# Optimization experiments

Measured on AMD Instinct MI355X. Metric: run time of the kernel, lower is better.

## Reference

```python
import jax, jax.numpy as jnp
import numpy as np
from jax import lax

PRE_NMS_THRESH = 0.05
PRE_NMS_TOP_N = 1000
FINAL_NMS_THRESH = 0.4  # hardcoded in forward(): boxlist_nms(..., 0.4)
MIN_SIZE = 0
STRIDE = 4.0
NEG = -1e9

N, C, H, W = 32, 1, 384, 384


def setup_inputs() -> dict:
    key = jax.random.key(0)
    k1, k2 = jax.random.split(key)
    box_cls = jax.random.uniform(k1, (N, C, H, W), dtype=jnp.float32)
    box_regression = jax.random.normal(k2, (N, 4, H, W), dtype=jnp.float32) * 20.0
    image_sizes = jnp.full((N, 2), H * int(STRIDE), dtype=jnp.int32)
    return {"box_cls": box_cls, "box_regression": box_regression, "image_sizes": image_sizes}


def decode_boxes(quad):
    # quad: [N, 4, H, W]; EAST geometry decode at stride 4 -> xyxy
    n, _, h, w = quad.shape
    x = (jnp.arange(w, dtype=quad.dtype) * STRIDE)[None, :]   # [1, W]
    y = (jnp.arange(h, dtype=quad.dtype) * STRIDE)[:, None]   # [H, 1]
    ymin = y - quad[:, 0]
    xmax = x + quad[:, 1]
    ymax = y + quad[:, 2]
    xmin = x - quad[:, 3]
    return jnp.stack([xmin, ymin, xmax, ymax], axis=1)  # [N, 4, H, W] (permute (3,0,1,2))


def iou_matrix(b):
    # b: [K, 4] xyxy
    x1, y1, x2, y2 = b[:, 0], b[:, 1], b[:, 2], b[:, 3]
    area = jnp.clip(x2 - x1, 0) * jnp.clip(y2 - y1, 0)
    ix1 = jnp.maximum(x1[:, None], x1[None, :])
    iy1 = jnp.maximum(y1[:, None], y1[None, :])
    ix2 = jnp.minimum(x2[:, None], x2[None, :])
    iy2 = jnp.minimum(y2[:, None], y2[None, :])
    inter = jnp.clip(ix2 - ix1, 0) * jnp.clip(iy2 - iy1, 0)
    union = area[:, None] + area[None, :] - inter
    return inter / jnp.maximum(union, 1e-9)


def greedy_nms(boxes, init_keep):
    # boxes: [K, 4] sorted by descending score; init_keep: [K] bool
    K = boxes.shape[0]
    iou = iou_matrix(boxes)
    idx = jnp.arange(K)

    def body(i, keep):
        suppress = (iou[i] > FINAL_NMS_THRESH) & (idx > i)
        return jnp.where(keep[i], keep & ~suppress, keep)

    return lax.fori_loop(0, K, body, init_keep)


def _forward(box_cls, box_regression):
    n, c, h, w = box_cls.shape
    boxes = decode_boxes(box_regression)                       # [N, 4, H, W]
    boxes = boxes.transpose(0, 2, 3, 1).reshape(n, h * w, 4)   # [N, HW, 4]
    scores = box_cls.transpose(0, 2, 3, 1).reshape(n, h * w)   # [N, HW] (C=1)

    # threshold + conditional top-k (padding with NEG emulates variable counts)
    masked = jnp.where(scores > PRE_NMS_THRESH, scores, NEG)
    scores_k, idx_k = lax.top_k(masked, PRE_NMS_TOP_N)         # [N, K], sorted desc
    boxes_k = jnp.take_along_axis(boxes, idx_k[..., None], axis=1)  # [N, K, 4]

    valid = scores_k > PRE_NMS_THRESH
    ws = boxes_k[..., 2] - boxes_k[..., 0]
    hs = boxes_k[..., 3] - boxes_k[..., 1]
    valid = valid & (ws >= MIN_SIZE) & (hs >= MIN_SIZE)        # remove_small_boxes

    keep = jax.vmap(greedy_nms)(boxes_k, valid)                # [N, K]
    out = jnp.concatenate([boxes_k, scores_k[..., None]], axis=-1)
    out = out * keep[..., None].astype(out.dtype)              # [N, K, 5]
    return out, keep


def reference(box_cls, box_regression, image_sizes):
    return _forward(box_cls, box_regression)
```

## Files before the change

kernel.cpp:

```cpp
#include <hip/hip_runtime.h>
#include <stdint.h>

#define NIMG 32
#define WID 384
#define HW 147456
#define TOPK 1000
#define KPAD 1024
#define NBINS 512
#define BIN_SCALEF 512.0f
#define SEGCAP 256
#define CANDCAP 2048
#define THRESH 0.05f
#define PREF_C 0.99f
#define NMS_T 0.4f
#define NBLK 18
#define FINEBINS 256

typedef unsigned long long u64;
typedef unsigned int u32;

#define PCNT_OFF 0
#define PCAND_OFF 4096

__device__ __forceinline__ float area_of(float x0, float y0, float x1, float y1) {
  float a = fmaxf(x1 - x0, 0.0f) * fmaxf(y1 - y0, 0.0f);
  asm volatile("" : "+v"(a));
  return a;
}

__device__ __forceinline__ bool iou_gt(float ax0, float ay0, float ax1, float ay1, float aa,
                                       float bx0, float by0, float bx1, float by1, float ba) {
  float ix1 = fmaxf(ax0, bx0);
  float iy1 = fmaxf(ay0, by0);
  float ix2 = fminf(ax1, bx1);
  float iy2 = fminf(ay1, by1);
  float iw = fmaxf(ix2 - ix1, 0.0f);
  float ih = fmaxf(iy2 - iy1, 0.0f);
  float inter = iw * ih;
  asm volatile("" : "+v"(inter));
  float uni = fmaxf(aa + ba - inter, 1e-9f);
  return (inter / uni) > NMS_T;
}

__device__ __forceinline__ u64 shflxor64(u64 v, int m) {
  int lo = __shfl_xor((int)(u32)v, m, 64);
  int hi = __shfl_xor((int)(u32)(v >> 32), m, 64);
  return ((u64)(u32)hi << 32) | (u32)lo;
}

__device__ __forceinline__ u64 make_key(float s, u32 idx) {
  u32 ord = __float_as_uint(s) | 0x80000000u;
  return ((u64)ord << 32) | (u32)(~idx);
}

__device__ __forceinline__ float score_of(u64 key) {
  return __uint_as_float((u32)(key >> 32) & 0x7FFFFFFFu);
}

__device__ __forceinline__ int bin_of(float s) {
  int b = (int)(s * BIN_SCALEF);
  return b < 0 ? 0 : (b > NBINS - 1 ? NBINS - 1 : b);
}

__device__ __forceinline__ int finebin(u64 key) {
  float s = score_of(key);
  int b = (int)((s - 0.99f) * 25600.0f);
  return b < 0 ? 0 : (b > FINEBINS - 1 ? FINEBINS - 1 : b);
}

__global__ __launch_bounds__(256) void scan_kernel(const float* __restrict__ cls,
                                                   u32* __restrict__ pcnt,
                                                   u64* __restrict__ pcand) {
  __shared__ u64 lbuf[SEGCAP];
  __shared__ u32 lcnt;
  const int n = blockIdx.y;
  const int tid = threadIdx.x;
  const int lane = tid & 63;
  if (tid == 0) lcnt = 0;
  __syncthreads();

  const float4* src = (const float4*)(cls + (size_t)n * HW) + blockIdx.x * 2048;
  float4 A[8];
#pragma unroll
  for (int v = 0; v < 8; v++) A[v] = src[tid + v * 256];

  const u64 ltmask = (1ull << lane) - 1ull;
#pragma unroll
  for (int v = 0; v < 8; v++) {
    float ss[4] = {A[v].x, A[v].y, A[v].z, A[v].w};
#pragma unroll
    for (int c = 0; c < 4; c++) {
      float s = ss[c];
      bool pc = s > PREF_C;
      u64 m = __ballot(pc);
      if (m) {
        int ldr = __ffsll(m) - 1;
        u32 wb = 0;
        if (lane == ldr) wb = atomicAdd(&lcnt, (u32)__popcll(m));
        wb = (u32)__shfl((int)wb, ldr, 64);
        if (pc) {
          u32 pos = wb + (u32)__popcll(m & ltmask);
          if (pos < SEGCAP) lbuf[pos] = make_key(s, (u32)((blockIdx.x * 2048 + tid + v * 256) * 4 + c));
        }
      }
    }
  }
  __syncthreads();
  const int seg = n * NBLK + blockIdx.x;
  if (tid == 0) pcnt[seg] = (lcnt > SEGCAP) ? 0xFFFFFFFFu : lcnt;
  u32 c = lcnt < SEGCAP ? lcnt : (u32)SEGCAP;
  u64* pc = pcand + (size_t)seg * SEGCAP;
  for (u32 i = tid; i < c; i += 256) pc[i] = lbuf[i];
}

#define REGCHAIN(K, JSTART) do {                                            \
    const bool desc_ = ((tid & ((K) >> 1)) == 0);                           \
    for (int j_ = (JSTART); j_ >= 2; j_ >>= 1) {                            \
      int h_ = j_ >> 1;                                                     \
      bool low_ = (tid & h_) == 0;                                          \
      u64 p0_ = shflxor64(e0, h_), p1_ = shflxor64(e1, h_);                 \
      bool tm_ = (low_ == desc_);                                           \
      e0 = tm_ ? (e0 > p0_ ? e0 : p0_) : (e0 < p0_ ? e0 : p0_);             \
      e1 = tm_ ? (e1 > p1_ ? e1 : p1_) : (e1 < p1_ ? e1 : p1_);             \
    }                                                                       \
    { u64 lo_ = e0 < e1 ? e0 : e1, hi_ = e0 < e1 ? e1 : e0;                 \
      e0 = desc_ ? hi_ : lo_; e1 = desc_ ? lo_ : hi_; }                     \
  } while (0)

__global__ __launch_bounds__(1024) void fused_kernel(const float* __restrict__ cls,
                                                     const float* __restrict__ reg,
                                                     const u32* __restrict__ pcnt,
                                                     const u64* __restrict__ pcand,
                                                     float* __restrict__ out) {
  __shared__ __align__(16) unsigned char smem[90112];
  u64* CKEY   = (u64*)smem;
  u32* BINNED = (u32*)(smem + 16384);
  u64* RKEY   = (u64*)(smem + 24576);
  float4* vbox  = (float4*)smem;
  float*  varea = (float*)(smem + 16384);
  u64*    mlds  = (u64*)(smem + 20480);

  __shared__ u32 BINSTART[FINEBINS + 1];
  __shared__ u32 HIST[FINEBINS];
  __shared__ u32 scnt[NBLK];
  __shared__ u32 soff[NBLK];
  __shared__ u32 bs[NBINS];
  __shared__ u32 stmp[64];
  __shared__ int stbin;
  __shared__ u32 sflag, sfc;
  __shared__ int sC;
  __shared__ u32 wcnt[16], woff[16];
  __shared__ int pc[136], pk[136];
  __shared__ int sV, snch, snp;
  __shared__ u64 keepsh[16], srem[16];

  const int n = blockIdx.x;
  const int tid = threadIdx.x;
  const int lane = tid & 63;
  const int w = tid >> 6;
  const u64 ltmask = (1ull << lane) - 1ull;

  if (tid < NBLK) scnt[tid] = pcnt[n * NBLK + tid];
  CKEY[tid] = 0ull; CKEY[tid + 1024] = 0ull;
  RKEY[tid] = 0ull;
  if (tid < FINEBINS) HIST[tid] = 0;
  if (tid == 0) sfc = 0;
  __syncthreads();
  if (tid == 0) {
    u32 f = 0, off = 0;
    for (int s = 0; s < NBLK; s++) {
      u32 c = scnt[s];
      if (c == 0xFFFFFFFFu) { f = 1; c = 0; }
      soff[s] = off; off += c;
    }
    if (off < TOPK || off > CANDCAP) f = 1;
    sflag = f; sC = (int)off;
  }
  __syncthreads();

  u64 key;

  if (sflag == 0) {
    const int C = sC;
    for (int seg = w; seg < NBLK; seg += 16) {
      u32 c = scnt[seg];
      u32 o = soff[seg];
      const u64* src2 = pcand + (size_t)(n * NBLK + seg) * SEGCAP;
      for (u32 i = lane; i < c; i += 64) CKEY[o + i] = src2[i];
    }
    __syncthreads();
    for (int i = tid; i < C; i += 1024) atomicAdd(&HIST[finebin(CKEY[i])], 1u);
    __syncthreads();
    if (tid < 64) {
      u32 h0 = HIST[lane * 4 + 0], h1 = HIST[lane * 4 + 1];
      u32 h2 = HIST[lane * 4 + 2], h3 = HIST[lane * 4 + 3];
      u32 t = h0 + h1 + h2 + h3;
      u32 incl = t;
#pragma unroll
      for (int d = 1; d < 64; d <<= 1) {
        u32 v = (u32)__shfl_up((int)incl, d, 64);
        if (lane >= d) incl += v;
      }
      u32 base = incl - t;
      BINSTART[lane * 4 + 0] = base;
      BINSTART[lane * 4 + 1] = base + h0;
      BINSTART[lane * 4 + 2] = base + h0 + h1;
      BINSTART[lane * 4 + 3] = base + h0 + h1 + h2;
      if (lane == 63) BINSTART[FINEBINS] = incl;
      HIST[lane * 4 + 0] = 0; HIST[lane * 4 + 1] = 0;
      HIST[lane * 4 + 2] = 0; HIST[lane * 4 + 3] = 0;
    }
    __syncthreads();
    for (int i = tid; i < C; i += 1024) {
      int bb = finebin(CKEY[i]);
      u32 slot = atomicAdd(&HIST[bb], 1u);
      BINNED[BINSTART[bb] + slot] = (u32)i;
    }
    __syncthreads();
    for (int i = tid; i < C; i += 1024) {
      u64 k = CKEY[i];
      int bb = finebin(k);
      u32 s0 = BINSTART[bb], s1 = BINSTART[bb + 1];
      u32 g = 0;
      for (u32 j = s0; j < s1; j++) {
        u32 cj = BINNED[j];
        if (CKEY[cj] > k) g++;
      }
      u32 rank = (u32)C - s1 + g;
      if (rank < KPAD) RKEY[rank] = k;
    }
    __syncthreads();
    key = RKEY[tid];
  } else {
    for (int i = tid; i < NBINS; i += 1024) bs[i] = 0;
    __syncthreads();
    const float* ci = cls + (size_t)n * HW;
    for (int base = 0; base < HW; base += 1024) {
      float s = ci[base + tid];
      if (s > THRESH) atomicAdd(&bs[bin_of(s)], 1u);
    }
    __syncthreads();
    if (tid < 64) {
      u32 cs = 0;
#pragma unroll
      for (int k2 = 0; k2 < 8; k2++) cs += bs[lane * 8 + k2];
      u32 s = cs;
#pragma unroll
      for (int d = 1; d < 64; d <<= 1) {
        u32 v = (u32)__shfl_down((int)s, d, 64);
        if (lane + d < 64) s += v;
      }
      stmp[lane] = s;
      u64 mask = __ballot(s >= TOPK);
      if (lane == 0) {
        int t = 0;
        if (mask) {
          int L = 63 - __clzll(mask);
          u32 acc = (L < 63) ? stmp[L + 1] : 0;
          for (int bb = L * 8 + 7; bb >= L * 8; bb--) {
            acc += bs[bb];
            if (acc >= TOPK) { t = bb; break; }
          }
        }
        stbin = t;
      }
    }
    __syncthreads();
    const int t = stbin;
    for (int base = 0; base < HW; base += 1024) {
      int i = base + tid;
      float s = ci[i];
      bool p = (s > THRESH) && (bin_of(s) >= t);
      u64 m = __ballot(p);
      if (m) {
        int ldr = __ffsll(m) - 1;
        u32 wb = 0;
        if (lane == ldr) wb = atomicAdd(&sfc, (u32)__popcll(m));
        wb = (u32)__shfl((int)wb, ldr, 64);
        if (p) { u32 pos = wb + (u32)__popcll(m & ltmask); if (pos < CANDCAP) CKEY[pos] = make_key(s, (u32)i); }
      }
    }
    __syncthreads();
    {
      u64 e0 = CKEY[2 * tid], e1 = CKEY[2 * tid + 1];
      REGCHAIN(2, 1); REGCHAIN(4, 2); REGCHAIN(8, 4); REGCHAIN(16, 8);
      REGCHAIN(32, 16); REGCHAIN(64, 32); REGCHAIN(128, 64);
      for (int k = 256; k <= CANDCAP; k <<= 1) {
        CKEY[2 * tid] = e0; CKEY[2 * tid + 1] = e1;
        __syncthreads();
        for (int j = k >> 1; j >= 128; j >>= 1) {
          int i = ((tid & ~(j - 1)) << 1) | (tid & (j - 1));
          u64 a = CKEY[i], bb = CKEY[i + j];
          bool desc = ((i & k) == 0);
          if (desc ? (a < bb) : (a > bb)) { CKEY[i] = bb; CKEY[i + j] = a; }
          __syncthreads();
        }
        e0 = CKEY[2 * tid]; e1 = CKEY[2 * tid + 1];
        REGCHAIN(k, 64);
      }
      CKEY[2 * tid] = e0; CKEY[2 * tid + 1] = e1;
      __syncthreads();
    }
    key = CKEY[tid];
  }

  float4 b = make_float4(0.f, 0.f, 0.f, 0.f);
  if (key != 0ull && tid < TOPK) {
    u32 idx = ~(u32)(key & 0xFFFFFFFFull);
    int iy = (int)idx / WID;
    int ix = (int)idx - iy * WID;
    float xx = (float)ix * 4.0f;
    float yy = (float)iy * 4.0f;
    const float* rb = reg + (size_t)n * 4 * HW;
    float r0 = rb[idx];
    float r1 = rb[HW + idx];
    float r2 = rb[2 * HW + idx];
    float r3 = rb[3 * HW + idx];
    b.y = yy - r0; b.z = xx + r1; b.w = yy + r2; b.x = xx - r3;
  }
  float s = score_of(key);
  __syncthreads();

  bool vb = (tid < TOPK) && (s > THRESH) && (b.z - b.x >= 0.0f) && (b.w - b.y >= 0.0f);
  vbox[tid] = make_float4(0.f, 0.f, 0.f, 0.f);
  varea[tid] = 0.0f;
  u64 vm = __ballot(vb);
  if (lane == 0) wcnt[w] = (u32)__popcll(vm);
  if (tid < 16) { srem[tid] = 0ull; keepsh[tid] = 0ull; }
  __syncthreads();
  if (tid == 0) {
    u32 off = 0;
    for (int i = 0; i < 16; i++) { woff[i] = off; off += wcnt[i]; }
    int V = (int)off;
    int nch = (V + 63) >> 6;
    sV = V; snch = nch; snp = nch * (nch + 1) / 2;
  }
  __syncthreads();
  const int V = sV, nch = snch, npairs = snp;

  int pos = -1;
  if (vb) {
    pos = (int)(woff[w] + (u32)__popcll(vm & ltmask));
    vbox[pos] = b;
    varea[pos] = area_of(b.x, b.y, b.z, b.w);
  }
  if (tid < npairs) {
    int p = tid, c = 0, base = 0;
    while (p >= base + (nch - c)) { base += nch - c; c++; }
    pc[tid] = c; pk[tid] = c + (p - base);
  }
  __syncthreads();

  for (int r = w; r < npairs * 64; r += 16) {
    int p = r >> 6, i = r & 63;
    int c = pc[p], k = pk[p];
    float4 rbx = vbox[k * 64 + i];
    float rarea = varea[k * 64 + i];
    float4 cbx = vbox[c * 64 + lane];
    float carea = varea[c * 64 + lane];
    bool pred = iou_gt(rbx.x, rbx.y, rbx.z, rbx.w, rarea,
                       cbx.x, cbx.y, cbx.z, cbx.w, carea);
    u64 m = __ballot(pred);
    if (lane == 0) mlds[r] = m;
  }
  __syncthreads();

  if (tid < 64) {
    for (int c = 0; c < nch; c++) {
      int pbase = c * nch - (c * (c - 1)) / 2 - c;
      u64 diag = mlds[(pbase + c) * 64 + lane];
      u64 ainit = (V >= (c + 1) * 64) ? ~0ull
                : ((V > c * 64) ? ((1ull << (V - c * 64)) - 1ull) : 0ull);
      u64 alive;
      {
        u64 a = ainit & ~srem[c];
        u32 alo2 = __builtin_amdgcn_readfirstlane((u32)a);
        u32 ahi2 = __builtin_amdgcn_readfirstlane((u32)(a >> 32));
        alive = ((u64)ahi2 << 32) | alo2;
      }
      u32 rlo = (u32)diag, rhi = (u32)(diag >> 32);
      u64 cur = alive;
      while (cur) {
        int i = __ffsll(cur) - 1;
        u32 rl = __builtin_amdgcn_readlane(rlo, i);
        u32 rh = __builtin_amdgcn_readlane(rhi, i);
        u64 rowi = ((u64)rh << 32) | rl;
        u64 lowmask = (i == 63) ? ~0ull : ((1ull << (i + 1)) - 1ull);
        rowi &= ~lowmask;
        alive &= ~rowi;
        cur &= ~rowi;
        cur &= cur - 1;
      }
      if (lane == 0) keepsh[c] = alive;
      const u64 K = alive;
      for (int k = c + 1; k < nch; k++) {
        bool sup = (mlds[(pbase + k) * 64 + lane] & K) != 0ull;
        u64 mres = __ballot(sup);
        if (lane == 0) srem[k] |= mres;
      }
    }
  }
  __syncthreads();

  u64 kb = (vb && pos >= 0) ? ((keepsh[pos >> 6] >> (pos & 63)) & 1ull) : 0ull;
  if (tid < TOPK) {
    float f = (float)kb;
    size_t ob = (size_t)n * (TOPK * 5) + (size_t)tid * 5;
    out[ob + 0] = kb ? b.x : 0.0f;
    out[ob + 1] = kb ? b.y : 0.0f;
    out[ob + 2] = kb ? b.z : 0.0f;
    out[ob + 3] = kb ? b.w : 0.0f;
    out[ob + 4] = kb ? s : 0.0f;
    out[(size_t)NIMG * TOPK * 5 + (size_t)n * TOPK + tid] = f;
  }
}

extern "C" void kernel_launch(void* const* d_in, const int* in_sizes, int n_in,
                              void* d_out, int out_size, void* d_ws, size_t ws_size,
                              hipStream_t stream) {
  const float* cls = (const float*)d_in[0];
  const float* reg = (const float*)d_in[1];
  float* out = (float*)d_out;

  uint8_t* ws = (uint8_t*)d_ws;
  u32* pcnt = (u32*)(ws + PCNT_OFF);
  u64* pcand = (u64*)(ws + PCAND_OFF);

  scan_kernel<<<dim3(NBLK, NIMG), 256, 0, stream>>>(cls, pcnt, pcand);
  fused_kernel<<<NIMG, 1024, 0, stream>>>(cls, reg, pcnt, pcand, out);
}
```

Before: 165.2 us.

## Decode candidate boxes in scan kernel and carry them through ranking

The box decode for each prefiltered candidate (four scattered reads of the regression tensor) moves from the single-block-per-image fused kernel into the wide scan kernel. The decoded boxes are written to a workspace buffer and carried alongside the keys through the rank scatter. This takes the dependent gather latency off the serial per-image critical path. It also halves the per-segment candidate capacity, which makes the fallback full-sort path more likely on inputs with dense high scores. The NMS box storage in shared memory changes from an array of float4 to four separate float arrays.

```diff
diff --git a/kernel.cpp b/kernel.cpp
--- a/kernel.cpp
+++ b/kernel.cpp
@@ -8,7 +8,7 @@
 #define KPAD 1024
 #define NBINS 512
 #define BIN_SCALEF 512.0f
-#define SEGCAP 256
+#define SEGCAP 128
 #define CANDCAP 2048
 #define THRESH 0.05f
 #define PREF_C 0.99f
@@ -21,6 +21,7 @@
 
 #define PCNT_OFF 0
 #define PCAND_OFF 4096
+#define PBOX_OFF  593920
 
 __device__ __forceinline__ float area_of(float x0, float y0, float x1, float y1) {
   float a = fmaxf(x1 - x0, 0.0f) * fmaxf(y1 - y0, 0.0f);
@@ -69,8 +70,10 @@
 }
 
 __global__ __launch_bounds__(256) void scan_kernel(const float* __restrict__ cls,
+                                                   const float* __restrict__ reg,
                                                    u32* __restrict__ pcnt,
-                                                   u64* __restrict__ pcand) {
+                                                   u64* __restrict__ pcand,
+                                                   float4* __restrict__ pbox) {
   __shared__ u64 lbuf[SEGCAP];
   __shared__ u32 lcnt;
   const int n = blockIdx.y;
@@ -109,8 +112,25 @@
   const int seg = n * NBLK + blockIdx.x;
   if (tid == 0) pcnt[seg] = (lcnt > SEGCAP) ? 0xFFFFFFFFu : lcnt;
   u32 c = lcnt < SEGCAP ? lcnt : (u32)SEGCAP;
-  u64* pc = pcand + (size_t)seg * SEGCAP;
-  for (u32 i = tid; i < c; i += 256) pc[i] = lbuf[i];
+  const float* rb = reg + (size_t)n * 4 * HW;
+  u64* pk = pcand + (size_t)seg * SEGCAP;
+  float4* pb = pbox + (size_t)seg * SEGCAP;
+  for (u32 i = tid; i < c; i += 256) {
+    u64 key = lbuf[i];
+    u32 idx = ~(u32)(key & 0xFFFFFFFFull);
+    int iy = (int)idx / WID;
+    int ix = (int)idx - iy * WID;
+    float xx = (float)ix * 4.0f;
+    float yy = (float)iy * 4.0f;
+    float r0 = rb[idx];
+    float r1 = rb[HW + idx];
+    float r2 = rb[2 * HW + idx];
+    float r3 = rb[3 * HW + idx];
+    float4 box;
+    box.y = yy - r0; box.z = xx + r1; box.w = yy + r2; box.x = xx - r3;
+    pk[i] = key;
+    pb[i] = box;
+  }
 }
 
 #define REGCHAIN(K, JSTART) do {                                            \
@@ -131,14 +151,20 @@
                                                      const float* __restrict__ reg,
                                                      const u32* __restrict__ pcnt,
                                                      const u64* __restrict__ pcand,
+                                                     const float4* __restrict__ pbox,
                                                      float* __restrict__ out) {
   __shared__ __align__(16) unsigned char smem[90112];
-  u64* CKEY   = (u64*)smem;
-  u32* BINNED = (u32*)(smem + 16384);
-  u64* RKEY   = (u64*)(smem + 24576);
-  float4* vbox  = (float4*)smem;
-  float*  varea = (float*)(smem + 16384);
-  u64*    mlds  = (u64*)(smem + 20480);
+  u64*    CKEY   = (u64*)smem;
+  float4* CBOX   = (float4*)(smem + 16384);
+  u32*    BINNED = (u32*)(smem + 49152);
+  u64*    RKEY   = (u64*)(smem + 57344);
+  float4* RBOX   = (float4*)(smem + 65536);
+  float* vx    = (float*)smem;
+  float* vy    = (float*)(smem + 4096);
+  float* vz    = (float*)(smem + 8192);
+  float* vw    = (float*)(smem + 12288);
+  float* varea = (float*)(smem + 16384);
+  u64*   mlds  = (u64*)(smem + 20480);
 
   __shared__ u32 BINSTART[FINEBINS + 1];
   __shared__ u32 HIST[FINEBINS];
@@ -161,7 +187,6 @@
   const u64 ltmask = (1ull << lane) - 1ull;
 
   if (tid < NBLK) scnt[tid] = pcnt[n * NBLK + tid];
-  CKEY[tid] = 0ull; CKEY[tid + 1024] = 0ull;
   RKEY[tid] = 0ull;
   if (tid < FINEBINS) HIST[tid] = 0;
   if (tid == 0) sfc = 0;
@@ -178,15 +203,19 @@
   }
   __syncthreads();
 
-  u64 key;
+  u64 key; float4 b;
 
   if (sflag == 0) {
     const int C = sC;
     for (int seg = w; seg < NBLK; seg += 16) {
       u32 c = scnt[seg];
       u32 o = soff[seg];
-      const u64* src2 = pcand + (size_t)(n * NBLK + seg) * SEGCAP;
-      for (u32 i = lane; i < c; i += 64) CKEY[o + i] = src2[i];
+      const u64* srck = pcand + (size_t)(n * NBLK + seg) * SEGCAP;
+      const float4* srcb = pbox + (size_t)(n * NBLK + seg) * SEGCAP;
+      for (u32 i = lane; i < c; i += 64) {
+        CKEY[o + i] = srck[i];
+        CBOX[o + i] = srcb[i];
+      }
     }
     __syncthreads();
     for (int i = tid; i < C; i += 1024) atomicAdd(&HIST[finebin(CKEY[i])], 1u);
@@ -227,12 +256,14 @@
         if (CKEY[cj] > k) g++;
       }
       u32 rank = (u32)C - s1 + g;
-      if (rank < KPAD) RKEY[rank] = k;
+      if (rank < KPAD) { RKEY[rank] = k; RBOX[rank] = CBOX[i]; }
     }
     __syncthreads();
     key = RKEY[tid];
+    b = (key != 0ull) ? RBOX[tid] : make_float4(0.f, 0.f, 0.f, 0.f);
   } else {
     for (int i = tid; i < NBINS; i += 1024) bs[i] = 0;
+    CKEY[tid] = 0ull; CKEY[tid + 1024] = 0ull;
     __syncthreads();
     const float* ci = cls + (size_t)n * HW;
     for (int base = 0; base < HW; base += 1024) {
@@ -302,27 +333,26 @@
       __syncthreads();
     }
     key = CKEY[tid];
-  }
-
-  float4 b = make_float4(0.f, 0.f, 0.f, 0.f);
-  if (key != 0ull && tid < TOPK) {
-    u32 idx = ~(u32)(key & 0xFFFFFFFFull);
-    int iy = (int)idx / WID;
-    int ix = (int)idx - iy * WID;
-    float xx = (float)ix * 4.0f;
-    float yy = (float)iy * 4.0f;
-    const float* rb = reg + (size_t)n * 4 * HW;
-    float r0 = rb[idx];
-    float r1 = rb[HW + idx];
-    float r2 = rb[2 * HW + idx];
-    float r3 = rb[3 * HW + idx];
-    b.y = yy - r0; b.z = xx + r1; b.w = yy + r2; b.x = xx - r3;
+    b = make_float4(0.f, 0.f, 0.f, 0.f);
+    if (key != 0ull && tid < TOPK) {
+      u32 idx = ~(u32)(key & 0xFFFFFFFFull);
+      int iy = (int)idx / WID;
+      int ix = (int)idx - iy * WID;
+      float xx = (float)ix * 4.0f;
+      float yy = (float)iy * 4.0f;
+      const float* rb = reg + (size_t)n * 4 * HW;
+      float r0 = rb[idx];
+      float r1 = rb[HW + idx];
+      float r2 = rb[2 * HW + idx];
+      float r3 = rb[3 * HW + idx];
+      b.y = yy - r0; b.z = xx + r1; b.w = yy + r2; b.x = xx - r3;
+    }
   }
   float s = score_of(key);
   __syncthreads();
 
   bool vb = (tid < TOPK) && (s > THRESH) && (b.z - b.x >= 0.0f) && (b.w - b.y >= 0.0f);
-  vbox[tid] = make_float4(0.f, 0.f, 0.f, 0.f);
+  vx[tid] = 0.0f; vy[tid] = 0.0f; vz[tid] = 0.0f; vw[tid] = 0.0f;
   varea[tid] = 0.0f;
   u64 vm = __ballot(vb);
   if (lane == 0) wcnt[w] = (u32)__popcll(vm);
@@ -341,7 +371,7 @@
   int pos = -1;
   if (vb) {
     pos = (int)(woff[w] + (u32)__popcll(vm & ltmask));
-    vbox[pos] = b;
+    vx[pos] = b.x; vy[pos] = b.y; vz[pos] = b.z; vw[pos] = b.w;
     varea[pos] = area_of(b.x, b.y, b.z, b.w);
   }
   if (tid < npairs) {
@@ -354,12 +384,11 @@
   for (int r = w; r < npairs * 64; r += 16) {
     int p = r >> 6, i = r & 63;
     int c = pc[p], k = pk[p];
-    float4 rbx = vbox[k * 64 + i];
-    float rarea = varea[k * 64 + i];
-    float4 cbx = vbox[c * 64 + lane];
-    float carea = varea[c * 64 + lane];
-    bool pred = iou_gt(rbx.x, rbx.y, rbx.z, rbx.w, rarea,
-                       cbx.x, cbx.y, cbx.z, cbx.w, carea);
+    int ri = k * 64 + i;
+    float rx0 = vx[ri], ry0 = vy[ri], rx1 = vz[ri], ry1 = vw[ri], ra = varea[ri];
+    int ci = c * 64 + lane;
+    float cx0 = vx[ci], cy0 = vy[ci], cx1 = vz[ci], cy1 = vw[ci], ca = varea[ci];
+    bool pred = iou_gt(rx0, ry0, rx1, ry1, ra, cx0, cy0, cx1, cy1, ca);
     u64 m = __ballot(pred);
     if (lane == 0) mlds[r] = m;
   }
@@ -425,7 +454,8 @@
   uint8_t* ws = (uint8_t*)d_ws;
   u32* pcnt = (u32*)(ws + PCNT_OFF);
   u64* pcand = (u64*)(ws + PCAND_OFF);
-
-  scan_kernel<<<dim3(NBLK, NIMG), 256, 0, stream>>>(cls, pcnt, pcand);
-  fused_kernel<<<NIMG, 1024, 0, stream>>>(cls, reg, pcnt, pcand, out);
-}
+  float4* pbox = (float4*)(ws + PBOX_OFF);
+
+  scan_kernel<<<dim3(NBLK, NIMG), 256, 0, stream>>>(cls, reg, pcnt, pcand, pbox);
+  fused_kernel<<<NIMG, 1024, 0, stream>>>(cls, reg, pcnt, pcand, pbox, out);
+}
```

New measurement: 154.9 us. 1.07x faster.
